# Kernel tuning notes

Measured on AMD Instinct MI355X. Metric: run time of the kernel, lower is better.

## Reference

```python
import jax, jax.numpy as jnp
import numpy as np


def setup_inputs() -> dict:
    key = jax.random.key(0)
    k1, k2 = jax.random.split(key)
    B, N, T, D = 4, 5000, 96, 64
    spatial_nodes = jax.random.normal(k1, (B, N, D), dtype=jnp.float32)
    temporal_nodes = jax.random.normal(k2, (B, T, D), dtype=jnp.float32)
    return {"spatial_nodes": spatial_nodes, "temporal_nodes": temporal_nodes}


def reference(spatial_nodes, temporal_nodes):
    # node_embs: [B, N+T, D]
    node_embs = jnp.concatenate([spatial_nodes, temporal_nodes], axis=1)
    # Gram matrix per batch: [B, N+T, N+T]
    adj = jax.nn.relu(jnp.einsum('bnf,bmf->bnm', node_embs, node_embs))
    M = node_embs.shape[1]
    eye = jnp.eye(M, dtype=adj.dtype)  # broadcast over batch instead of repeat
    adj = jnp.tanh(adj + eye)
    # NOTE: the torch original additionally extracts per-batch edge lists via
    # adj[bi].nonzero() — a data-dependent-shape compaction that is not
    # jit-expressible; the dense adj carries identical information
    # (edge (i,j) exists iff adj[b,i,j] != 0, weight = adj[b,i,j]).
    return adj
```

## Files before the change

### kernel.cpp

```cpp
#include <hip/hip_runtime.h>


#define NSP 5000
#define NTM 96
#define MM  5096
#define DD  64
#define BT  128
#define NTILE 40

typedef __attribute__((ext_vector_type(8))) short short8;
typedef __attribute__((ext_vector_type(8))) unsigned short ushort8;
typedef __attribute__((ext_vector_type(4))) float f32x4;

__device__ __forceinline__ unsigned short bf16_rn(float x) {
  unsigned u = __float_as_uint(x);
  u += 0x7FFFu + ((u >> 16) & 1u);
  return (unsigned short)(u >> 16);
}
__device__ __forceinline__ float bf16_f32(unsigned short s) {
  return __uint_as_float(((unsigned)s) << 16);
}

__global__ __launch_bounds__(256) void stg_prep_kernel(
    const float* __restrict__ sp, const float* __restrict__ tm,
    unsigned short* __restrict__ wsh, unsigned short* __restrict__ wsl) {
  const int tid = blockIdx.x * 256 + threadIdx.x;
  const int flat = tid * 8;
  const int b = flat / (MM * DD);
  const int rem = flat - b * (MM * DD);
  const int m = rem / DD;
  const int d = rem - m * DD;
  const float* src = (m < NSP)
      ? sp + ((size_t)b * NSP + m) * DD + d
      : tm + ((size_t)b * NTM + (m - NSP)) * DD + d;
  const float4* s4 = reinterpret_cast<const float4*>(src);
  float f[8];
  {
    float4 v0 = s4[0], v1 = s4[1];
    f[0]=v0.x; f[1]=v0.y; f[2]=v0.z; f[3]=v0.w;
    f[4]=v1.x; f[5]=v1.y; f[6]=v1.z; f[7]=v1.w;
  }
  ushort8 H, L;
  #pragma unroll
  for (int i = 0; i < 8; ++i) {
    const unsigned short hi = bf16_rn(f[i]);
    H[i] = hi;
    L[i] = bf16_rn(f[i] - bf16_f32(hi));
  }
  *reinterpret_cast<ushort8*>(wsh + flat) = H;
  *reinterpret_cast<ushort8*>(wsl + flat) = L;
}

__global__ __launch_bounds__(256, 2) void stg_adj_kernel(
    const unsigned short* __restrict__ wsh,
    const unsigned short* __restrict__ wsl,
    float* __restrict__ out) {
  __shared__ unsigned char lds[65536];
  const int bi = blockIdx.x;
  const int bj = blockIdx.y;
  const int b  = blockIdx.z;
  const int t  = threadIdx.x;

  const size_t pb = (size_t)b * MM * DD;

  #pragma unroll
  for (int comp = 0; comp < 4; ++comp) {
    const int tbase = (comp < 2 ? bi : bj) * BT;
    const unsigned short* src = ((comp & 1) ? wsl : wsh) + pb;
    unsigned char* dst = lds + comp * 16384;
    #pragma unroll
    for (int k = 0; k < 4; ++k) {
      const int G = t + k * 256;
      const int row = G >> 3;
      const int g = G & 7;
      int grow = tbase + row; grow = grow < MM ? grow : MM - 1;
      const ushort8 v = *reinterpret_cast<const ushort8*>(src + (size_t)grow * DD + g * 8);
      *reinterpret_cast<ushort8*>(dst + row * 128 + ((g ^ (row & 7)) << 4)) = v;
    }
  }
  __syncthreads();

  const int lane = t & 63;
  const int wave = t >> 6;
  const int wr = (wave >> 1) << 6;
  const int wc = (wave & 1) << 6;
  const int lr = lane & 15;
  const int lg = lane >> 4;

  f32x4 acc[4][4];
  #pragma unroll
  for (int m = 0; m < 4; ++m)
    #pragma unroll
    for (int n = 0; n < 4; ++n)
      acc[m][n] = (f32x4){0.f, 0.f, 0.f, 0.f};

  #pragma unroll
  for (int ks = 0; ks < 2; ++ks) {
    short8 ah[4], al[4], ch[4], cl[4];
    #pragma unroll
    for (int m = 0; m < 4; ++m) {
      const int ra = wr + m * 16 + lr;
      const unsigned ga = (unsigned)((lg + ks * 4) ^ (ra & 7)) << 4;
      ah[m] = *reinterpret_cast<short8*>(lds +         ra * 128 + ga);
      al[m] = *reinterpret_cast<short8*>(lds + 16384 + ra * 128 + ga);
      const int rc = wc + m * 16 + lr;
      const unsigned gc_ = (unsigned)((lg + ks * 4) ^ (rc & 7)) << 4;
      ch[m] = *reinterpret_cast<short8*>(lds + 32768 + rc * 128 + gc_);
      cl[m] = *reinterpret_cast<short8*>(lds + 49152 + rc * 128 + gc_);
    }
    #pragma unroll
    for (int m = 0; m < 4; ++m) {
      #pragma unroll
      for (int n = 0; n < 4; ++n) {
        acc[m][n] = __builtin_amdgcn_mfma_f32_16x16x32_bf16(ch[n], ah[m], acc[m][n], 0, 0, 0);
        acc[m][n] = __builtin_amdgcn_mfma_f32_16x16x32_bf16(ch[n], al[m], acc[m][n], 0, 0, 0);
        acc[m][n] = __builtin_amdgcn_mfma_f32_16x16x32_bf16(cl[n], ah[m], acc[m][n], 0, 0, 0);
      }
    }
  }

  const size_t cbase = (size_t)b * MM * MM;
  const int gr0 = bi * BT + wr;
  const int gc0 = bj * BT + wc;
  #pragma unroll
  for (int m = 0; m < 4; ++m) {
    const int gr = gr0 + m * 16 + lr;
    if (gr < MM) {
      float* rowp = out + cbase + (size_t)gr * MM;
      #pragma unroll
      for (int n = 0; n < 4; ++n) {
        const int gc = gc0 + n * 16 + lg * 4;
        if (gc < MM) {
          f32x4 v;
          #pragma unroll
          for (int q = 0; q < 4; ++q) {
            float xv = fmaxf(acc[m][n][q], 0.f);
            xv += (gr == gc + q) ? 1.f : 0.f;
            const float e = __builtin_amdgcn_exp2f(xv * 2.8853900817779268f);
            v[q] = 1.f - 2.f * __builtin_amdgcn_rcpf(e + 1.f);
          }
          *reinterpret_cast<f32x4*>(rowp + gc) = v;
        }
      }
    }
  }
}

extern "C" void kernel_launch(void* const* d_in, const int* in_sizes, int n_in,
                              void* d_out, int out_size, void* d_ws, size_t ws_size,
                              hipStream_t stream) {
  const float* sp = (const float*)d_in[0];
  const float* tm = (const float*)d_in[1];
  float* out = (float*)d_out;
  const int B = in_sizes[0] / (NSP * DD);
  unsigned short* wsh = (unsigned short*)d_ws;
  unsigned short* wsl = wsh + (size_t)B * MM * DD;

  const int prep_threads = B * MM * DD / 8;
  stg_prep_kernel<<<dim3(prep_threads / 256), dim3(256), 0, stream>>>(sp, tm, wsh, wsl);

  dim3 grid(NTILE, NTILE, B);
  stg_adj_kernel<<<grid, dim3(256), 0, stream>>>(wsh, wsl, out);
}
```

Baseline: 109.2 us.

## Exploit Gram symmetry: compute upper-triangle tiles and mirror-store transposes

```diff
diff --git a/kernel.cpp b/kernel.cpp
--- a/kernel.cpp
+++ b/kernel.cpp
@@ -6,7 +6,7 @@
 #define MM  5096
 #define DD  64
 #define BT  128
-#define NTILE 40
+#define NTRI 820
 
 typedef __attribute__((ext_vector_type(8))) short short8;
 typedef __attribute__((ext_vector_type(8))) unsigned short ushort8;
@@ -56,17 +56,25 @@
     const unsigned short* __restrict__ wsl,
     float* __restrict__ out) {
   __shared__ unsigned char lds[65536];
-  const int bi = blockIdx.x;
-  const int bj = blockIdx.y;
-  const int b  = blockIdx.z;
-  const int t  = threadIdx.x;
-
+  const int p = blockIdx.x;
+  const int b = blockIdx.y;
+
+  int bi = (int)((81.0f - sqrtf(6561.0f - 8.0f * (float)p)) * 0.5f);
+  bi = bi < 0 ? 0 : (bi > 39 ? 39 : bi);
+  while (bi > 0 && bi * (81 - bi) / 2 > p) --bi;
+  while ((bi + 1) * (81 - (bi + 1)) / 2 <= p) ++bi;
+  const int bj = bi + (p - bi * (81 - bi) / 2);
+  const bool diag = (bi == bj);
+
+  const int t = threadIdx.x;
   const size_t pb = (size_t)b * MM * DD;
-
-  #pragma unroll
-  for (int comp = 0; comp < 4; ++comp) {
+  const unsigned short* Xh = wsh + pb;
+  const unsigned short* Xl = wsl + pb;
+
+  const int npanel = diag ? 2 : 4;
+  for (int comp = 0; comp < npanel; ++comp) {
     const int tbase = (comp < 2 ? bi : bj) * BT;
-    const unsigned short* src = ((comp & 1) ? wsl : wsh) + pb;
+    const unsigned short* src = (comp & 1) ? Xl : Xh;
     unsigned char* dst = lds + comp * 16384;
     #pragma unroll
     for (int k = 0; k < 4; ++k) {
@@ -87,6 +95,9 @@
   const int lr = lane & 15;
   const int lg = lane >> 4;
 
+  unsigned char* chb = diag ? lds : (lds + 32768);
+  unsigned char* clb = chb + 16384;
+
   f32x4 acc[4][4];
   #pragma unroll
   for (int m = 0; m < 4; ++m)
@@ -105,8 +116,8 @@
       al[m] = *reinterpret_cast<short8*>(lds + 16384 + ra * 128 + ga);
       const int rc = wc + m * 16 + lr;
       const unsigned gc_ = (unsigned)((lg + ks * 4) ^ (rc & 7)) << 4;
-      ch[m] = *reinterpret_cast<short8*>(lds + 32768 + rc * 128 + gc_);
-      cl[m] = *reinterpret_cast<short8*>(lds + 49152 + rc * 128 + gc_);
+      ch[m] = *reinterpret_cast<short8*>(chb + rc * 128 + gc_);
+      cl[m] = *reinterpret_cast<short8*>(clb + rc * 128 + gc_);
     }
     #pragma unroll
     for (int m = 0; m < 4; ++m) {
@@ -119,9 +130,35 @@
     }
   }
 
-  const size_t cbase = (size_t)b * MM * MM;
   const int gr0 = bi * BT + wr;
   const int gc0 = bj * BT + wc;
+  #pragma unroll
+  for (int m = 0; m < 4; ++m)
+    #pragma unroll
+    for (int n = 0; n < 4; ++n)
+      #pragma unroll
+      for (int q = 0; q < 4; ++q)
+        acc[m][n][q] = fmaxf(acc[m][n][q], 0.f);
+  if (diag) {
+    #pragma unroll
+    for (int m = 0; m < 4; ++m)
+      #pragma unroll
+      for (int n = 0; n < 4; ++n)
+        #pragma unroll
+        for (int q = 0; q < 4; ++q)
+          if ((gr0 + m * 16 + lr) == (gc0 + n * 16 + lg * 4 + q)) acc[m][n][q] += 1.f;
+  }
+  #pragma unroll
+  for (int m = 0; m < 4; ++m)
+    #pragma unroll
+    for (int n = 0; n < 4; ++n)
+      #pragma unroll
+      for (int q = 0; q < 4; ++q) {
+        const float e = __builtin_amdgcn_exp2f(acc[m][n][q] * 2.8853900817779268f);
+        acc[m][n][q] = 1.f - 2.f * __builtin_amdgcn_rcpf(e + 1.f);
+      }
+
+  const size_t cbase = (size_t)b * MM * MM;
   #pragma unroll
   for (int m = 0; m < 4; ++m) {
     const int gr = gr0 + m * 16 + lr;
@@ -130,16 +167,25 @@
       #pragma unroll
       for (int n = 0; n < 4; ++n) {
         const int gc = gc0 + n * 16 + lg * 4;
-        if (gc < MM) {
-          f32x4 v;
+        if (gc < MM)
+          *reinterpret_cast<f32x4*>(rowp + gc) = acc[m][n];
+      }
+    }
+  }
+
+  if (!diag) {
+    #pragma unroll
+    for (int n = 0; n < 4; ++n) {
+      #pragma unroll
+      for (int q = 0; q < 4; ++q) {
+        const int rowg = gc0 + n * 16 + lg * 4 + q;
+        if (rowg < MM) {
+          float* rowp = out + cbase + (size_t)rowg * MM;
           #pragma unroll
-          for (int q = 0; q < 4; ++q) {
-            float xv = fmaxf(acc[m][n][q], 0.f);
-            xv += (gr == gc + q) ? 1.f : 0.f;
-            const float e = __builtin_amdgcn_exp2f(xv * 2.8853900817779268f);
-            v[q] = 1.f - 2.f * __builtin_amdgcn_rcpf(e + 1.f);
+          for (int m = 0; m < 4; ++m) {
+            const int colg = gr0 + m * 16 + lr;
+            if (colg < MM) rowp[colg] = acc[m][n][q];
           }
-          *reinterpret_cast<f32x4*>(rowp + gc) = v;
         }
       }
     }
@@ -159,6 +205,5 @@
   const int prep_threads = B * MM * DD / 8;
   stg_prep_kernel<<<dim3(prep_threads / 256), dim3(256), 0, stream>>>(sp, tm, wsh, wsl);
 
-  dim3 grid(NTILE, NTILE, B);
-  stg_adj_kernel<<<grid, dim3(256), 0, stream>>>(wsh, wsl, out);
-}
+  stg_adj_kernel<<<dim3(NTRI, B), dim3(256), 0, stream>>>(wsh, wsl, out);
+}
```

New measurement: 132.8 us. +21.6%, slower.
